# Optimization experiments

Measured on AMD Instinct MI355X. Metric: run time of the kernel, lower is better.

The kernel has to match this reference:

```python
import jax, jax.numpy as jnp
import numpy as np

SIZE = 14          # feature-map side (448 image / stride 32)
IMG_STRIDE = 32    # feature->image coordinate stride
RATIOS = [(4, 4), (3, 5), (5, 3), (6, 6), (5, 7), (7, 5), (8, 8), (6, 10), (10, 6)]
GROUPS = [(0, 3), (3, 6), (6, 9)]   # ratio index ranges per scale group
N_LIST = [3, 2, 1]                   # proposals kept per group (sum = proposalN = 6)
IOU_THRESHS = [0.25, 0.25, 0.25]
WIN_NUMS = [(SIZE - h + 1) * (SIZE - w + 1) for h, w in RATIOS]  # 121,120,120,81,80,80,49,45,45
OFFS = np.cumsum([0] + WIN_NUMS)


def _make_coords():
    # image-space [x0,y0,x1,y1] per window, same order as flattened avgpool outputs
    coords = []
    for h, w in RATIOS:
        Ho, Wo = SIZE - h + 1, SIZE - w + 1
        for i in range(Ho):
            for j in range(Wo):
                x0 = i * IMG_STRIDE - 1
                y0 = j * IMG_STRIDE - 1
                x1 = x0 + h * IMG_STRIDE
                y1 = y0 + w * IMG_STRIDE
                coords.append([max(x0, 0), max(y0, 0), x1, y1])
    return np.asarray(coords, np.int32)  # [741, 4]


def setup_inputs() -> dict:
    key = jax.random.key(0)
    B = 65536
    x = jax.random.normal(key, (B, 1, SIZE, SIZE), dtype=jnp.float32)
    coords = jnp.asarray(_make_coords())
    return {"x": x, "coords": coords, "proposalN": 6}


def _avgpool_scores(x):
    # x: [B,1,H,W] -> concat of flattened VALID avgpools, [B, sum(WIN_NUMS)]
    B = x.shape[0]
    outs = []
    for h, w in RATIOS:
        s = jax.lax.reduce_window(x, 0.0, jax.lax.add, (1, 1, h, w), (1, 1, 1, 1), 'VALID')
        outs.append((s / (h * w)).reshape(B, -1))
    return jnp.concatenate(outs, axis=1)


def _nms_group(scores, coords_f, areas, N, thresh):
    # greedy NMS: repeatedly take argmax of remaining scores, suppress IoU>thresh.
    # Matches the torch/numpy loop (sorted-walk == repeated argmax for distinct scores).
    W = scores.shape[0]
    def step(carry, _):
        mask, last = carry
        any_v = jnp.any(mask)
        idx = jnp.argmax(jnp.where(mask, scores, -jnp.inf)).astype(jnp.int32)
        idx = jnp.where(any_v, idx, last)  # if exhausted, repeat last pick (as original)
        c = coords_f[idx]
        lx = jnp.minimum(coords_f[:, 2], c[2]) - jnp.maximum(coords_f[:, 0], c[0]) + 1.0
        ly = jnp.minimum(coords_f[:, 3], c[3]) - jnp.maximum(coords_f[:, 1], c[1]) + 1.0
        inter = jnp.where((lx < 0) | (ly < 0), 0.0, lx * ly)
        iou = inter / (areas + areas[idx] - inter)
        return (mask & (iou <= thresh), idx), idx
    init = (jnp.ones((W,), dtype=bool), jnp.int32(0))
    _, idxs = jax.lax.scan(step, init, None, length=N)
    return idxs  # [N] int32


def reference(x, coords, proposalN):
    all_scores = _avgpool_scores(x)                 # [B, 741]
    coords_f = coords.astype(jnp.float32)
    areas = (coords_f[:, 2] - coords_f[:, 0] + 1.0) * (coords_f[:, 3] - coords_f[:, 1] + 1.0)
    idx_parts = []
    for g, (a, b) in enumerate(GROUPS):
        s, e = int(OFFS[a]), int(OFFS[b])
        cf, ar = coords_f[s:e], areas[s:e]
        N, t = N_LIST[g], IOU_THRESHS[g]
        f = lambda sc, cf=cf, ar=ar, N=N, t=t: _nms_group(sc, cf, ar, N, t)
        idx_parts.append(jax.vmap(f)(all_scores[:, s:e]) + s)  # [B, N]
    proposalN_indices = jnp.concatenate(idx_parts, axis=1)      # [B, proposalN]
    proposalN_windows_scores = jnp.take_along_axis(all_scores, proposalN_indices, axis=1)
    window_scores = all_scores
    return proposalN_indices, proposalN_windows_scores, window_scores
```

## Files before the change

kernel.cpp:

```cpp
#include <hip/hip_runtime.h>
#include <stdint.h>
#include <math.h>

#define NW 741
#define NEG_INF_KEY 0x007FFFFFu

__device__ __forceinline__ unsigned score_key(float f) {
  const unsigned u = __float_as_uint(f);
  return (u & 0x80000000u) ? ~u : (u | 0x80000000u);
}
__device__ __forceinline__ float key_score(unsigned k) {
  return __uint_as_float((k & 0x80000000u) ? (k ^ 0x80000000u) : ~k);
}

template<int CTRL>
__device__ __forceinline__ void argmax_step(unsigned& k, int& i) {
  const unsigned tk = (unsigned)__builtin_amdgcn_update_dpp(0, (int)k, CTRL, 0xF, 0xF, true);
  const int ti = __builtin_amdgcn_update_dpp(0, i, CTRL, 0xF, 0xF, true);
  if (tk > k || (tk == k && ti < i)) { k = tk; i = ti; }
}
__device__ __forceinline__ void wave_argmax(unsigned& k, int& i) {
  argmax_step<0x111>(k, i);
  argmax_step<0x112>(k, i);
  argmax_step<0x114>(k, i);
  argmax_step<0x118>(k, i);
  argmax_step<0x142>(k, i);
  argmax_step<0x143>(k, i);
  k = (unsigned)__builtin_amdgcn_readlane((int)k, 63);
  i = __builtin_amdgcn_readlane(i, 63);
}

template<int H, int W, int OFF>
__device__ __forceinline__ void score_ratio2(const float2* __restrict__ im2,
                                             unsigned* __restrict__ wk2,
                                             float* __restrict__ wrowA,
                                             float* __restrict__ wrowB,
                                             const int lane, const bool hasB) {
  constexpr int Wo = 14 - W + 1;
  constexpr int Ho = 14 - H + 1;
  constexpr int NWIN = Ho * Wo;
  for (int o = lane; o < NWIN; o += 64) {
    const int i = o / Wo, j = o - i * Wo;
    const float2* p = im2 + (i * 14 + j);
    float2 acc; acc.x = 0.0f; acc.y = 0.0f;
#pragma unroll
    for (int di = 0; di < H; ++di)
#pragma unroll
      for (int dj = 0; dj < W; ++dj) {
        const float2 v = p[di * 14 + dj];
        acc.x += v.x; acc.y += v.y;
      }
    const float scA = acc.x / (float)(H * W);
    const float scB = acc.y / (float)(H * W);
    wrowA[OFF + o] = scA;
    if (hasB) wrowB[OFF + o] = scB;
    uint2 kk; kk.x = score_key(scA); kk.y = score_key(scB);
    *(uint2*)&wk2[(OFF + o) * 2] = kk;
  }
}

__global__ __launch_bounds__(256) void appm_kernel(
    const float* __restrict__ x, const int* __restrict__ coords,
    float* __restrict__ out, int B) {

  __shared__ float4 c_box[NW];
  __shared__ float c_ar[NW];
  __shared__ float imgp[4][392];
  __shared__ unsigned wkk[4][NW * 2];

  const int t = threadIdx.x;
  const int wv = t >> 6;
  const int lane = t & 63;
  const int img0 = blockIdx.x * 8;
  const int imgA = img0 + wv * 2;
  const int imgB = imgA + 1;
  const bool hasA = (imgA < B);
  const bool hasB = (imgB < B);

  for (int w = t; w < NW; w += 256) {
    const int4 c = ((const int4*)coords)[w];
    const float fx0 = (float)c.x, fy0 = (float)c.y;
    const float fx1 = (float)c.z, fy1 = (float)c.w;
    c_box[w] = make_float4(fx0, fy0, fx1, fy1);
    c_ar[w] = (fx1 - fx0 + 1.0f) * (fy1 - fy0 + 1.0f);
  }

  {
    int nimg = B - img0; if (nimg > 8) nimg = 8;
    const int lim = nimg * 196;
    const float* xb = x + (long long)img0 * 196;
    for (int u = t; u < lim; u += 256) {
      const int i = u / 196, k = u - i * 196;
      imgp[i >> 1][k * 2 + (i & 1)] = xb[u];
    }
  }
  __syncthreads();

  if (hasA) {
    const float2* im2 = (const float2*)imgp[wv];
    unsigned* wk2 = wkk[wv];
    float* wrowA = out + (long long)B * 12 + (long long)imgA * NW;
    float* wrowB = wrowA + NW;

    score_ratio2<4, 4, 0>(im2, wk2, wrowA, wrowB, lane, hasB);
    score_ratio2<3, 5, 121>(im2, wk2, wrowA, wrowB, lane, hasB);
    score_ratio2<5, 3, 241>(im2, wk2, wrowA, wrowB, lane, hasB);
    score_ratio2<6, 6, 361>(im2, wk2, wrowA, wrowB, lane, hasB);
    score_ratio2<5, 7, 442>(im2, wk2, wrowA, wrowB, lane, hasB);
    score_ratio2<7, 5, 522>(im2, wk2, wrowA, wrowB, lane, hasB);
    score_ratio2<8, 8, 602>(im2, wk2, wrowA, wrowB, lane, hasB);
    score_ratio2<6, 10, 651>(im2, wk2, wrowA, wrowB, lane, hasB);
    score_ratio2<10, 6, 696>(im2, wk2, wrowA, wrowB, lane, hasB);
    __builtin_amdgcn_wave_barrier();

    float myIA = 0.0f, mySA = 0.0f, myIB = 0.0f, mySB = 0.0f;
    int pick = 0;
    constexpr int gs_[3] = {0, 361, 602};
    constexpr int ge_[3] = {361, 602, 741};
    constexpr int gn_[3] = {3, 2, 1};
#pragma unroll
    for (int g = 0; g < 3; g++) {
      const int gs = gs_[g], ge = ge_[g];
      int lastA = gs, lastB = gs;
      float lastSA = 0.0f, lastSB = 0.0f;
#pragma unroll
      for (int n = 0; n < gn_[g]; n++) {
        unsigned bkA = 0u, bkB = 0u;
        int biA = 0, biB = 0;
        for (int o = gs + lane; o < ge; o += 64) {
          const uint2 kk = *(const uint2*)&wkk[wv][o * 2];
          if (kk.x > bkA) { bkA = kk.x; biA = o; }
          if (kk.y > bkB) { bkB = kk.y; biB = o; }
        }
        wave_argmax(bkA, biA);
        wave_argmax(bkB, biB);

        int idxA, idxB; float scA, scB;
        if (bkA > NEG_INF_KEY) { idxA = biA; scA = key_score(bkA); }
        else { idxA = lastA; scA = lastSA; }
        if (bkB > NEG_INF_KEY) { idxB = biB; scB = key_score(bkB); }
        else { idxB = lastB; scB = lastSB; }
        lastA = idxA; lastSA = scA;
        lastB = idxB; lastSB = scB;
        if (lane == pick) { myIA = (float)idxA; mySA = scA; myIB = (float)idxB; mySB = scB; }
        pick++;

        if (n + 1 < gn_[g]) {
          const float4 bA = c_box[idxA]; const float aA = c_ar[idxA];
          const float4 bB = c_box[idxB]; const float aB = c_ar[idxB];
          for (int o = gs + lane; o < ge; o += 64) {
            const float4 cb = c_box[o];
            const float ar = c_ar[o];
            const float lxA = fminf(cb.z, bA.z) - fmaxf(cb.x, bA.x) + 1.0f;
            const float lyA = fminf(cb.w, bA.w) - fmaxf(cb.y, bA.y) + 1.0f;
            const float inA = (lxA < 0.0f || lyA < 0.0f) ? 0.0f : lxA * lyA;
            const bool supA = (4.0f * inA > ar + aA - inA);
            const float lxB = fminf(cb.z, bB.z) - fmaxf(cb.x, bB.x) + 1.0f;
            const float lyB = fminf(cb.w, bB.w) - fmaxf(cb.y, bB.y) + 1.0f;
            const float inB = (lxB < 0.0f || lyB < 0.0f) ? 0.0f : lxB * lyB;
            const bool supB = (4.0f * inB > ar + aB - inB);
            uint2 kk = *(uint2*)&wkk[wv][o * 2];
            if (supA) kk.x = 0u;
            if (supB) kk.y = 0u;
            *(uint2*)&wkk[wv][o * 2] = kk;
          }
          __builtin_amdgcn_wave_barrier();
        }
      }
    }

    if (lane < 6) {
      const long long a6 = (long long)imgA * 6 + lane;
      out[a6] = myIA;
      out[(long long)B * 6 + a6] = mySA;
      if (hasB) {
        const long long b6 = (long long)imgB * 6 + lane;
        out[b6] = myIB;
        out[(long long)B * 6 + b6] = mySB;
      }
    }
  }
}

extern "C" void kernel_launch(void* const* d_in, const int* in_sizes, int n_in,
                              void* d_out, int out_size, void* d_ws, size_t ws_size,
                              hipStream_t stream) {
  const float* x = (const float*)d_in[0];
  const int* coords = (const int*)d_in[1];
  float* out = (float*)d_out;
  const int B = in_sizes[0] / 196;
  const int nblk = (B + 7) / 8;
  appm_kernel<<<dim3(nblk), dim3(256), 0, stream>>>(x, coords, out, B);
}
```

Baseline: 442.9 us.

## Keep NMS score keys in registers and replicate image tiles to cut LDS conflicts

Each lane now keeps its window score keys in fixed register slots (15 per image) instead of a per-wave LDS array, so the argmax and suppression loops are fully unrolled and read no shared memory. The image tile in LDS is stored four times, and each window reads from a copy chosen by its position, to spread LDS bank accesses. Launch bounds now request occupancy 4. The cost is higher register pressure and a larger, four-fold replicated image store during staging.

```diff
diff --git a/kernel.cpp b/kernel.cpp
--- a/kernel.cpp
+++ b/kernel.cpp
@@ -1,9 +1,10 @@
 #include <hip/hip_runtime.h>
 #include <stdint.h>
-#include <math.h>
 
 #define NW 741
 #define NEG_INF_KEY 0x007FFFFFu
+
+typedef float f2 __attribute__((ext_vector_type(2)));
 
 __device__ __forceinline__ unsigned score_key(float f) {
   const unsigned u = __float_as_uint(f);
@@ -30,43 +31,50 @@
   i = __builtin_amdgcn_readlane(i, 63);
 }
 
-template<int H, int W, int OFF>
-__device__ __forceinline__ void score_ratio2(const float2* __restrict__ im2,
-                                             unsigned* __restrict__ wk2,
+template<int H, int W, int OFF, int NS, int SB>
+__device__ __forceinline__ void score_ratio2(const f2* __restrict__ im2,
+                                             unsigned* __restrict__ kA,
+                                             unsigned* __restrict__ kB,
                                              float* __restrict__ wrowA,
                                              float* __restrict__ wrowB,
                                              const int lane, const bool hasB) {
   constexpr int Wo = 14 - W + 1;
   constexpr int Ho = 14 - H + 1;
   constexpr int NWIN = Ho * Wo;
-  for (int o = lane; o < NWIN; o += 64) {
-    const int i = o / Wo, j = o - i * Wo;
-    const float2* p = im2 + (i * 14 + j);
-    float2 acc; acc.x = 0.0f; acc.y = 0.0f;
-#pragma unroll
-    for (int di = 0; di < H; ++di)
-#pragma unroll
-      for (int dj = 0; dj < W; ++dj) {
-        const float2 v = p[di * 14 + dj];
-        acc.x += v.x; acc.y += v.y;
-      }
-    const float scA = acc.x / (float)(H * W);
-    const float scB = acc.y / (float)(H * W);
-    wrowA[OFF + o] = scA;
-    if (hasB) wrowB[OFF + o] = scB;
-    uint2 kk; kk.x = score_key(scA); kk.y = score_key(scB);
-    *(uint2*)&wk2[(OFF + o) * 2] = kk;
-  }
-}
-
-__global__ __launch_bounds__(256) void appm_kernel(
+  constexpr int P = Wo + 2;
+#pragma unroll
+  for (int s = 0; s < NS; ++s) {
+    const int o = lane + 64 * s;
+    unsigned ka = 0u, kb = 0u;
+    if (o < NWIN) {
+      const int i = o / Wo, j = o - i * Wo;
+      const int cp = (o / P) & 3;
+      const f2* p = im2 + cp * 196 + (i * 14 + j);
+      f2 acc = {0.0f, 0.0f};
+#pragma unroll
+      for (int di = 0; di < H; ++di)
+#pragma unroll
+        for (int dj = 0; dj < W; ++dj)
+          acc += p[di * 14 + dj];
+      const float scA = acc.x / (float)(H * W);
+      const float scB = acc.y / (float)(H * W);
+      wrowA[OFF + o] = scA;
+      if (hasB) wrowB[OFF + o] = scB;
+      ka = score_key(scA);
+      kb = score_key(scB);
+    }
+    kA[SB + s] = ka;
+    kB[SB + s] = kb;
+  }
+}
+
+__global__ __launch_bounds__(256, 4) void appm_kernel(
     const float* __restrict__ x, const int* __restrict__ coords,
     float* __restrict__ out, int B) {
 
   __shared__ float4 c_box[NW];
   __shared__ float c_ar[NW];
-  __shared__ float imgp[4][392];
-  __shared__ unsigned wkk[4][NW * 2];
+  __shared__ f2 imgp[4][784];
 
   const int t = threadIdx.x;
   const int wv = t >> 6;
@@ -91,46 +99,55 @@
     const float* xb = x + (long long)img0 * 196;
     for (int u = t; u < lim; u += 256) {
       const int i = u / 196, k = u - i * 196;
-      imgp[i >> 1][k * 2 + (i & 1)] = xb[u];
+      const float v = xb[u];
+      float* dst = (float*)imgp[i >> 1];
+      const int fi = k * 2 + (i & 1);
+#pragma unroll
+      for (int cp = 0; cp < 4; ++cp)
+        dst[cp * 392 + fi] = v;
     }
   }
   __syncthreads();
 
   if (hasA) {
-    const float2* im2 = (const float2*)imgp[wv];
-    unsigned* wk2 = wkk[wv];
+    const f2* im2 = imgp[wv];
     float* wrowA = out + (long long)B * 12 + (long long)imgA * NW;
     float* wrowB = wrowA + NW;
 
-    score_ratio2<4, 4, 0>(im2, wk2, wrowA, wrowB, lane, hasB);
-    score_ratio2<3, 5, 121>(im2, wk2, wrowA, wrowB, lane, hasB);
-    score_ratio2<5, 3, 241>(im2, wk2, wrowA, wrowB, lane, hasB);
-    score_ratio2<6, 6, 361>(im2, wk2, wrowA, wrowB, lane, hasB);
-    score_ratio2<5, 7, 442>(im2, wk2, wrowA, wrowB, lane, hasB);
-    score_ratio2<7, 5, 522>(im2, wk2, wrowA, wrowB, lane, hasB);
-    score_ratio2<8, 8, 602>(im2, wk2, wrowA, wrowB, lane, hasB);
-    score_ratio2<6, 10, 651>(im2, wk2, wrowA, wrowB, lane, hasB);
-    score_ratio2<10, 6, 696>(im2, wk2, wrowA, wrowB, lane, hasB);
-    __builtin_amdgcn_wave_barrier();
+    unsigned kA[15], kB[15];
+
+    score_ratio2<4, 4, 0, 2, 0>(im2, kA, kB, wrowA, wrowB, lane, hasB);
+    score_ratio2<3, 5, 121, 2, 2>(im2, kA, kB, wrowA, wrowB, lane, hasB);
+    score_ratio2<5, 3, 241, 2, 4>(im2, kA, kB, wrowA, wrowB, lane, hasB);
+    score_ratio2<6, 6, 361, 2, 6>(im2, kA, kB, wrowA, wrowB, lane, hasB);
+    score_ratio2<5, 7, 442, 2, 8>(im2, kA, kB, wrowA, wrowB, lane, hasB);
+    score_ratio2<7, 5, 522, 2, 10>(im2, kA, kB, wrowA, wrowB, lane, hasB);
+    score_ratio2<8, 8, 602, 1, 12>(im2, kA, kB, wrowA, wrowB, lane, hasB);
+    score_ratio2<6, 10, 651, 1, 13>(im2, kA, kB, wrowA, wrowB, lane, hasB);
+    score_ratio2<10, 6, 696, 1, 14>(im2, kA, kB, wrowA, wrowB, lane, hasB);
+
+    constexpr int SBASE[15] = {0, 64, 121, 185, 241, 305, 361, 425,
+                               442, 506, 522, 586, 602, 651, 696};
+    constexpr int GS[3] = {0, 6, 12};
+    constexpr int GE[3] = {6, 12, 15};
+    constexpr int GN[3] = {3, 2, 1};
+    constexpr int GW0[3] = {0, 361, 602};
 
     float myIA = 0.0f, mySA = 0.0f, myIB = 0.0f, mySB = 0.0f;
     int pick = 0;
-    constexpr int gs_[3] = {0, 361, 602};
-    constexpr int ge_[3] = {361, 602, 741};
-    constexpr int gn_[3] = {3, 2, 1};
-#pragma unroll
-    for (int g = 0; g < 3; g++) {
-      const int gs = gs_[g], ge = ge_[g];
-      int lastA = gs, lastB = gs;
+#pragma unroll
+    for (int g = 0; g < 3; ++g) {
+      int lastA = GW0[g], lastB = GW0[g];
       float lastSA = 0.0f, lastSB = 0.0f;
 #pragma unroll
-      for (int n = 0; n < gn_[g]; n++) {
+      for (int n = 0; n < GN[g]; ++n) {
         unsigned bkA = 0u, bkB = 0u;
         int biA = 0, biB = 0;
-        for (int o = gs + lane; o < ge; o += 64) {
-          const uint2 kk = *(const uint2*)&wkk[wv][o * 2];
-          if (kk.x > bkA) { bkA = kk.x; biA = o; }
-          if (kk.y > bkB) { bkB = kk.y; biB = o; }
+#pragma unroll
+        for (int s = GS[g]; s < GE[g]; ++s) {
+          const int o = SBASE[s] + lane;
+          if (kA[s] > bkA) { bkA = kA[s]; biA = o; }
+          if (kB[s] > bkB) { bkB = kB[s]; biB = o; }
         }
         wave_argmax(bkA, biA);
         wave_argmax(bkB, biB);
@@ -145,12 +162,15 @@
         if (lane == pick) { myIA = (float)idxA; mySA = scA; myIB = (float)idxB; mySB = scB; }
         pick++;
 
-        if (n + 1 < gn_[g]) {
+        if (n + 1 < GN[g]) {
           const float4 bA = c_box[idxA]; const float aA = c_ar[idxA];
           const float4 bB = c_box[idxB]; const float aB = c_ar[idxB];
-          for (int o = gs + lane; o < ge; o += 64) {
-            const float4 cb = c_box[o];
-            const float ar = c_ar[o];
+#pragma unroll
+          for (int s = GS[g]; s < GE[g]; ++s) {
+            const int o = SBASE[s] + lane;
+            const int oc = (o < NW) ? o : (NW - 1);
+            const float4 cb = c_box[oc];
+            const float ar = c_ar[oc];
             const float lxA = fminf(cb.z, bA.z) - fmaxf(cb.x, bA.x) + 1.0f;
             const float lyA = fminf(cb.w, bA.w) - fmaxf(cb.y, bA.y) + 1.0f;
             const float inA = (lxA < 0.0f || lyA < 0.0f) ? 0.0f : lxA * lyA;
@@ -159,12 +179,9 @@
             const float lyB = fminf(cb.w, bB.w) - fmaxf(cb.y, bB.y) + 1.0f;
             const float inB = (lxB < 0.0f || lyB < 0.0f) ? 0.0f : lxB * lyB;
             const bool supB = (4.0f * inB > ar + aB - inB);
-            uint2 kk = *(uint2*)&wkk[wv][o * 2];
-            if (supA) kk.x = 0u;
-            if (supB) kk.y = 0u;
-            *(uint2*)&wkk[wv][o * 2] = kk;
+            if (supA) kA[s] = 0u;
+            if (supB) kB[s] = 0u;
           }
-          __builtin_amdgcn_wave_barrier();
         }
       }
     }
```

New measurement: 399.5 us. 9.8% less time.
